# Optimization experiments

Hardware: AMD Instinct MI355X
Metric: run time of the kernel (lower is better)

## Reference

```python
import jax, jax.numpy as jnp
import numpy as np

D_MODEL = 1024
N_HEADS = 16
D_K = D_MODEL // N_HEADS  # 64
THETA = 10000.0


def _rope(x, token_positions):
    # x: [b, h, s, d], token_positions: [s]
    inv_freq = 1.0 / THETA ** (jnp.arange(0, D_K, 2, dtype=jnp.float32) / D_K)  # [d/2]
    ang = token_positions.astype(jnp.float32)[:, None] * inv_freq               # [s, d/2]
    cos, sin = jnp.cos(ang), jnp.sin(ang)                                       # broadcast over b,h
    x1 = x[..., 0::2]
    x2 = x[..., 1::2]
    even = x1 * cos - x2 * sin
    odd = x1 * sin + x2 * cos
    return jnp.stack([even, odd], axis=-1).reshape(x.shape)  # re-interleave


def setup_inputs() -> dict:
    key = jax.random.key(0)
    k1, k2, k3 = jax.random.split(key, 3)
    B, S = 2, 2048
    x = jax.random.normal(k1, (B, S, D_MODEL), dtype=jnp.float32)
    token_positions = jnp.arange(S, dtype=jnp.int32)
    std_qkv = np.sqrt(2.0 / (D_MODEL + 3 * D_MODEL))
    std_out = np.sqrt(2.0 / (D_MODEL + D_MODEL))
    W_qkv = jax.random.normal(k2, (3 * D_MODEL, D_MODEL), dtype=jnp.float32) * std_qkv
    W_out = jax.random.normal(k3, (D_MODEL, D_MODEL), dtype=jnp.float32) * std_out
    return {"x": x, "token_positions": token_positions, "W_qkv": W_qkv, "W_out": W_out}


def reference(x, token_positions, W_qkv, W_out):
    B, S, _ = x.shape
    qkv = jnp.einsum('bsi,oi->bso', x, W_qkv)                 # [b, s, 3*h*d]
    qkv = qkv.reshape(B, S, 3, N_HEADS, D_K)
    qkv = jnp.transpose(qkv, (2, 0, 3, 1, 4))                 # [3, b, h, s, d]
    q, k, v = qkv[0], qkv[1], qkv[2]
    q = _rope(q, token_positions)
    k = _rope(k, token_positions)
    scores = jnp.einsum('bhqd,bhkd->bhqk', q, k) / jnp.sqrt(jnp.float32(D_K))
    mask = jnp.tril(jnp.ones((S, S), dtype=bool))
    scores = jnp.where(mask, scores, -jnp.inf)
    attn = jax.nn.softmax(scores, axis=-1)
    out = jnp.einsum('bhqk,bhkd->bhqd', attn, v)              # [b, h, s, d]
    out = jnp.transpose(out, (0, 2, 1, 3)).reshape(B, S, D_MODEL)
    return jnp.einsum('bsi,oi->bso', out, W_out)
```

## Files before the change

kernel.cpp:

```cpp
#include <hip/hip_runtime.h>
#include <hip/hip_bf16.h>
#include <math.h>

#define D_MODEL 1024
#define N_HEADS 16
#define D_K     64
#define S_LEN   2048
#define B_SZ    2

typedef unsigned short u16;
typedef unsigned int   u32;
using short8  = __attribute__((ext_vector_type(8))) short;
using ushort8 = __attribute__((ext_vector_type(8))) unsigned short;
using f32x4   = __attribute__((ext_vector_type(4))) float;

__device__ inline float bf2f(u16 u) { return __uint_as_float((u32)u << 16); }
__device__ inline u16 f2bf(float f) {
    __hip_bfloat16 h = __float2bfloat16(f);
    return *(u16*)&h;
}
__device__ inline void gload_lds16(const void* g, void* l) {
    __builtin_amdgcn_global_load_lds(
        (const __attribute__((address_space(1))) unsigned int*)g,
        (__attribute__((address_space(3))) unsigned int*)l, 16, 0, 0);
}

__global__ __launch_bounds__(256)
void cast3_f32_bf16(const float* __restrict__ a, u16* __restrict__ ao, int na4,
                    const float* __restrict__ bsrc, u16* __restrict__ bo, int nb4,
                    const float* __restrict__ c, u16* __restrict__ co, int nc4) {
    int j = blockIdx.x * 256 + threadIdx.x;
    const float* src; u16* dst;
    if (j < na4) { src = a; dst = ao; }
    else {
        j -= na4;
        if (j < nb4) { src = bsrc; dst = bo; }
        else {
            j -= nb4;
            if (j >= nc4) return;
            src = c; dst = co;
        }
    }
    float4 v = ((const float4*)src)[j];
    ushort4 u;
    u.x = f2bf(v.x); u.y = f2bf(v.y); u.z = f2bf(v.z); u.w = f2bf(v.w);
    ((ushort4*)dst)[j] = u;
}

template <bool OUT_BF16>
__global__ __launch_bounds__(256)
void gemm_bt_mfma(const u16* __restrict__ A, const u16* __restrict__ B,
                  void* __restrict__ Cout, int M, int N, int K) {
    __shared__ u16 As[128 * 32];
    __shared__ u16 Bs[128 * 32];
    const int tid  = threadIdx.x;
    const int lane = tid & 63;
    const int wv   = tid >> 6;
    const int wm   = wv >> 1, wn = wv & 1;
    const int row0 = blockIdx.y * 128;
    const int col0 = blockIdx.x * 128;

    const int lr = lane >> 2;
    const int lc = (lane & 3) * 8;

    f32x4 acc[4][4] = {};

    for (int k0 = 0; k0 < K; k0 += 32) {
#pragma unroll
        for (int t = 0; t < 2; t++) {
            int rblk = wv * 32 + t * 16;
            gload_lds16(A + (size_t)(row0 + rblk + lr) * K + k0 + lc, &As[rblk * 32]);
            gload_lds16(B + (size_t)(col0 + rblk + lr) * K + k0 + lc, &Bs[rblk * 32]);
        }
        __syncthreads();

        short8 af[4], bfr[4];
#pragma unroll
        for (int mi = 0; mi < 4; mi++)
            af[mi] = *(const short8*)&As[(wm * 64 + mi * 16 + (lane & 15)) * 32 + (lane >> 4) * 8];
#pragma unroll
        for (int nj = 0; nj < 4; nj++)
            bfr[nj] = *(const short8*)&Bs[(wn * 64 + nj * 16 + (lane & 15)) * 32 + (lane >> 4) * 8];
#pragma unroll
        for (int mi = 0; mi < 4; mi++)
#pragma unroll
            for (int nj = 0; nj < 4; nj++)
                acc[mi][nj] = __builtin_amdgcn_mfma_f32_16x16x32_bf16(
                    af[mi], bfr[nj], acc[mi][nj], 0, 0, 0);
        __syncthreads();
    }

    const int cr = (lane >> 4) * 4;
    const int cc = lane & 15;
#pragma unroll
    for (int mi = 0; mi < 4; mi++) {
#pragma unroll
        for (int nj = 0; nj < 4; nj++) {
            int c = col0 + wn * 64 + nj * 16 + cc;
#pragma unroll
            for (int r = 0; r < 4; r++) {
                int rr = row0 + wm * 64 + mi * 16 + cr + r;
                if (OUT_BF16)
                    ((u16*)Cout)[(size_t)rr * N + c] = f2bf(acc[mi][nj][r]);
                else
                    ((float*)Cout)[(size_t)rr * N + c] = acc[mi][nj][r];
            }
        }
    }
}

__global__ __launch_bounds__(256)
void prep_vtrans_rope(u16* __restrict__ qkv, u16* __restrict__ VT,
                      const int* __restrict__ pos) {
    const int bid = blockIdx.x;
    const int tid = threadIdx.x;

    if (bid < 1024) {
        __shared__ u16 t[64][68];
        const int st = bid & 31, h = (bid >> 5) & 15, b = bid >> 9;
        const int bh = b * N_HEADS + h;
#pragma unroll
        for (int i = 0; i < 4; i++) {
            int e  = tid + i * 256;
            int sl = e >> 4;
            int c4 = e & 15;
            ushort4 v = *(const ushort4*)&qkv[((size_t)(b * S_LEN + st * 64 + sl) * 3 + 2) * D_MODEL
                                              + h * D_K + c4 * 4];
            *(ushort4*)&t[sl][c4 * 4] = v;
        }
        __syncthreads();
#pragma unroll
        for (int i = 0; i < 4; i++) {
            int e  = tid + i * 256;
            int d  = e >> 4;
            int s4 = e & 15;
            ushort4 o;
            o.x = t[s4 * 4 + 0][d];
            o.y = t[s4 * 4 + 1][d];
            o.z = t[s4 * 4 + 2][d];
            o.w = t[s4 * 4 + 3][d];
            *(ushort4*)&VT[((size_t)bh * D_K + d) * S_LEN + st * 64 + s4 * 4] = o;
        }
        return;
    }

    int e  = (bid - 1024) * 256 + tid;
    int j8 = e & 7;
    int h  = (e >> 3) & 15;
    int w  = (e >> 7) & 1;
    int s  = (e >> 8) & 2047;
    int b  = e >> 19;

    float p  = (float)pos[s];
    float sc = (w == 0) ? 0.125f : 1.0f;

    size_t base = (((size_t)(b * S_LEN + s) * 3 + w) * D_MODEL) + h * D_K + j8 * 8;
    ushort8 v = *(const ushort8*)&qkv[base];

    const float C = -0.41524101186092056f;
#pragma unroll
    for (int jj = 0; jj < 4; jj++) {
        int j = j8 * 4 + jj;
        float ang = p * exp2f((float)j * C);
        float sn, cs;
        __sincosf(ang, &sn, &cs);
        float x1 = bf2f(v[2 * jj]);
        float x2 = bf2f(v[2 * jj + 1]);
        v[2 * jj]     = f2bf((x1 * cs - x2 * sn) * sc);
        v[2 * jj + 1] = f2bf((x1 * sn + x2 * cs) * sc);
    }
    *(ushort8*)&qkv[base] = v;
}

__device__ __forceinline__ void attn_step(
    const u16* __restrict__ Ksc, const u16* __restrict__ Vsc,
    u16* __restrict__ Psw,
    short8 (&qf)[2], f32x4 (&acc)[4], float& mq, float& lq,
    int k0, int qw0, bool diag, int l15, int quad, int qsw)
{
    f32x4 s[4] = {};
    __builtin_amdgcn_s_setprio(1);
#pragma unroll
    for (int kf = 0; kf < 2; kf++)
#pragma unroll
        for (int nj = 0; nj < 4; nj++) {
            short8 kfr = *(const short8*)&Ksc[kf * 2048 + (nj * 16 + l15) * 32 + qsw * 8];
            s[nj] = __builtin_amdgcn_mfma_f32_16x16x32_bf16(kfr, qf[kf], s[nj], 0, 0, 0);
        }
    __builtin_amdgcn_s_setprio(0);

    if (diag) {
        const int row_g = qw0 + l15;
#pragma unroll
        for (int nj = 0; nj < 4; nj++)
#pragma unroll
            for (int r = 0; r < 4; r++) {
                int key_g = k0 + nj * 16 + quad * 4 + r;
                if (key_g > row_g) s[nj][r] = -INFINITY;
            }
    }

    float rmax = s[0][0];
#pragma unroll
    for (int nj = 0; nj < 4; nj++)
#pragma unroll
        for (int r = 0; r < 4; r++) rmax = fmaxf(rmax, s[nj][r]);
    rmax = fmaxf(rmax, __shfl_xor(rmax, 16, 64));
    rmax = fmaxf(rmax, __shfl_xor(rmax, 32, 64));

    if (!__all(rmax <= mq + 8.f)) {
        float mn = fmaxf(mq, rmax);
        float alpha = __expf(mq - mn);
        mq = mn;
        lq *= alpha;
#pragma unroll
        for (int nj = 0; nj < 4; nj++)
#pragma unroll
            for (int r = 0; r < 4; r++) acc[nj][r] *= alpha;
    }

    float rsum = 0.f;
#pragma unroll
    for (int nj = 0; nj < 4; nj++)
#pragma unroll
        for (int r = 0; r < 4; r++) {
            float p = __expf(s[nj][r] - mq);
            s[nj][r] = p;
            rsum += p;
        }
    rsum += __shfl_xor(rsum, 16, 64);
    rsum += __shfl_xor(rsum, 32, 64);
    lq += rsum;

#pragma unroll
    for (int nj = 0; nj < 4; nj++) {
        u32 lo = ((u32)f2bf(s[nj][1]) << 16) | f2bf(s[nj][0]);
        u32 hi = ((u32)f2bf(s[nj][3]) << 16) | f2bf(s[nj][2]);
        uint2 pk; pk.x = lo; pk.y = hi;
        *(uint2*)&Psw[l15 * 68 + nj * 16 + quad * 4] = pk;
    }

    __builtin_amdgcn_s_setprio(1);
#pragma unroll
    for (int kf = 0; kf < 2; kf++) {
        const u16* pp = &Psw[l15 * 68 + kf * 32 + quad * 8];
        uint2 plo = *(const uint2*)pp;
        uint2 phi = *(const uint2*)(pp + 4);
        u32 praw[4] = { plo.x, plo.y, phi.x, phi.y };
        short8 pf = *(const short8*)praw;
#pragma unroll
        for (int nj = 0; nj < 4; nj++) {
            short8 vf = *(const short8*)&Vsc[kf * 2048 + (nj * 16 + l15) * 32 + qsw * 8];
            acc[nj] = __builtin_amdgcn_mfma_f32_16x16x32_bf16(vf, pf, acc[nj], 0, 0, 0);
        }
    }
    __builtin_amdgcn_s_setprio(0);
}

__global__ __launch_bounds__(256)
void attn_mfma(const u16* __restrict__ qkv, const u16* __restrict__ VT,
               u16* __restrict__ out, float* __restrict__ partO,
               float* __restrict__ partML) {
    __shared__ u16 Ks[2][64 * 32];
    __shared__ u16 VsT[2][64 * 32];
    __shared__ u16 Ps[4][16 * 68];

    const int tid  = threadIdx.x;
    const int lane = tid & 63;
    const int wv   = tid >> 6;

    const int bid  = blockIdx.x;
    const int idx  = bid >> 3;
    const int bh   = (bid & 7) * 4 + (idx >> 5);
    const int rem  = idx & 31;
    const int pr   = rem >> 1;
    const int role = rem & 1;
    const int qtH  = 31 - pr;
    const int qtL  = pr;
    const int h    = bh & (N_HEADS - 1);
    const int b    = bh >> 4;

    const int l15  = lane & 15;
    const int quad = lane >> 4;
    const int qsw  = quad ^ ((l15 >> 1) & 3);
    const int qw0H = qtH * 64 + wv * 16;

    const size_t vtb = (size_t)bh * D_K * S_LEN;
    u16* Psw = &Ps[wv][0];
    const int lr  = lane >> 2;
    const int csw = ((lane & 3) ^ ((lane >> 3) & 3)) * 8;

    auto STAGE = [&](int kts) {
        const int k0s = kts * 64;
#pragma unroll
        for (int kf = 0; kf < 2; kf++)
            gload_lds16(qkv + ((size_t)(b * S_LEN + k0s + wv * 16 + lr) * 3 + 1) * D_MODEL
                            + h * D_K + kf * 32 + csw,
                        &Ks[kf][(wv * 16) * 32]);
#pragma unroll
        for (int kc = 0; kc < 2; kc++)
            gload_lds16(VT + vtb + (size_t)(wv * 16 + lr) * S_LEN + k0s + kc * 32 + csw,
                        &VsT[kc][(wv * 16) * 32]);
    };

    short8 qfH[2];
#pragma unroll
    for (int kf = 0; kf < 2; kf++)
        qfH[kf] = *(const short8*)&qkv[((size_t)(b * S_LEN + qw0H + l15) * 3 + 0) * D_MODEL
                                       + h * D_K + kf * 32 + quad * 8];
    f32x4 accH[4] = {};
    float mqH = -INFINITY, lqH = 0.f;

    const int kbeg = role ? 17 : 0;
    const int kend = role ? qtH : 16;
    for (int kt = kbeg; kt <= kend; kt++) {
        STAGE(kt);
        __syncthreads();
        attn_step(&Ks[0][0], &VsT[0][0], Psw, qfH, accH, mqH, lqH,
                  kt * 64, qw0H, kt == qtH, l15, quad, qsw);
        __syncthreads();
    }

    {
        const size_t unit = (size_t)(bh * 16 + (qtH - 16)) * 2 + role;
        float* Od = partO + unit * 4096 + (size_t)(wv * 16 + l15) * 64;
#pragma unroll
        for (int nj = 0; nj < 4; nj++)
            *(f32x4*)&Od[nj * 16 + quad * 4] = accH[nj];
        if (quad == 0) {
            float* ML = partML + unit * 128;
            ML[wv * 16 + l15]      = mqH;
            ML[64 + wv * 16 + l15] = lqH;
        }
    }

    if (!role) return;

    const int qw0L = qtL * 64 + wv * 16;
    short8 qfL[2];
#pragma unroll
    for (int kf = 0; kf < 2; kf++)
        qfL[kf] = *(const short8*)&qkv[((size_t)(b * S_LEN + qw0L + l15) * 3 + 0) * D_MODEL
                                       + h * D_K + kf * 32 + quad * 8];
    f32x4 accL[4] = {};
    float mqL = -INFINITY, lqL = 0.f;

    for (int kt = 0; kt <= qtL; kt++) {
        STAGE(kt);
        __syncthreads();
        attn_step(&Ks[0][0], &VsT[0][0], Psw, qfL, accL, mqL, lqL,
                  kt * 64, qw0L, kt == qtL, l15, quad, qsw);
        __syncthreads();
    }

    float invl = 1.f / lqL;
#pragma unroll
    for (int nj = 0; nj < 4; nj++) {
        ushort4 o;
        o.x = f2bf(accL[nj][0] * invl); o.y = f2bf(accL[nj][1] * invl);
        o.z = f2bf(accL[nj][2] * invl); o.w = f2bf(accL[nj][3] * invl);
        *(ushort4*)&out[(size_t)(b * S_LEN + qw0L + l15) * D_MODEL
                        + h * D_K + nj * 16 + quad * 4] = o;
    }
}

__global__ __launch_bounds__(256)
void attn_combine(const float* __restrict__ partO, const float* __restrict__ partML,
                  u16* __restrict__ out) {
    const int t16 = blockIdx.x & 15;
    const int bh  = blockIdx.x >> 4;
    const int h = bh & (N_HEADS - 1), b = bh >> 4;
    const int q0 = (t16 + 16) * 64;
    const int tid = threadIdx.x;
    const int q  = tid >> 2;
    const int d0 = (tid & 3) * 16;

    const size_t u0 = (size_t)(bh * 16 + t16) * 2;
    const float* O0 = partO + u0 * 4096;
    const float* O1 = O0 + 4096;
    const float* ML0 = partML + u0 * 128;
    const float* ML1 = ML0 + 128;

    float m0 = ML0[q], l0 = ML0[64 + q];
    float m1 = ML1[q], l1 = ML1[64 + q];
    float ms = fmaxf(m0, m1);
    float f0 = __expf(m0 - ms), f1 = __expf(m1 - ms);
    float inv = 1.f / (l0 * f0 + l1 * f1);
    f0 *= inv; f1 *= inv;
#pragma unroll
    for (int i = 0; i < 4; i++) {
        float4 a = *(const float4*)&O0[q * 64 + d0 + i * 4];
        float4 c = *(const float4*)&O1[q * 64 + d0 + i * 4];
        ushort4 o;
        o.x = f2bf(a.x * f0 + c.x * f1);
        o.y = f2bf(a.y * f0 + c.y * f1);
        o.z = f2bf(a.z * f0 + c.z * f1);
        o.w = f2bf(a.w * f0 + c.w * f1);
        *(ushort4*)&out[(size_t)(b * S_LEN + q0 + q) * D_MODEL + h * D_K + d0 + i * 4] = o;
    }
}

extern "C" void kernel_launch(void* const* d_in, const int* in_sizes, int n_in,
                              void* d_out, int out_size, void* d_ws, size_t ws_size,
                              hipStream_t stream) {
    const float* x    = (const float*)d_in[0];
    const int*   pos  = (const int*)d_in[1];
    const float* Wqkv = (const float*)d_in[2];
    const float* Wout = (const float*)d_in[3];
    float*       out  = (float*)d_out;

    const int M = B_SZ * S_LEN;

    u16* qkvb = (u16*)d_ws;
    u16* aob  = qkvb + (size_t)M * 3 * D_MODEL;
    u16* xb   = aob  + (size_t)M * D_MODEL;
    u16* wqb  = xb   + (size_t)M * D_MODEL;
    u16* wob  = wqb  + (size_t)3 * D_MODEL * D_MODEL;
    u16* vtb  = wob  + (size_t)D_MODEL * D_MODEL;
    float* partO  = (float*)(vtb + (size_t)M * D_MODEL);
    float* partML = partO + (size_t)1024 * 4096;

    const int na4 = M * D_MODEL / 4;
    const int nb4 = 3 * D_MODEL * D_MODEL / 4;
    const int nc4 = D_MODEL * D_MODEL / 4;
    cast3_f32_bf16<<<(na4 + nb4 + nc4 + 255) / 256, 256, 0, stream>>>(
        x, xb, na4, Wqkv, wqb, nb4, Wout, wob, nc4);

    gemm_bt_mfma<true><<<dim3(3 * D_MODEL / 128, M / 128), 256, 0, stream>>>(
        xb, wqb, qkvb, M, 3 * D_MODEL, D_MODEL);

    prep_vtrans_rope<<<5120, 256, 0, stream>>>(qkvb, vtb, pos);

    attn_mfma<<<1024, 256, 0, stream>>>(qkvb, vtb, aob, partO, partML);
    attn_combine<<<512, 256, 0, stream>>>(partO, partML, aob);

    gemm_bt_mfma<false><<<dim3(D_MODEL / 128, M / 128), 256, 0, stream>>>(
        aob, wob, out, M, D_MODEL, D_MODEL);
}
```

Baseline: 197.6 us.

## Prefetch K/V tiles via registers, use exp2 softmax, smaller-tile output GEMM

The attention loop now prefetches the next K and V tiles into registers while computing the current tile, then writes them to LDS, instead of staging synchronously before each step. Softmax switches to base-2 exponentials, with the log2(e) factor folded into the Q scale, and the rescale threshold is raised from 8 to 12. The output projection uses a new 64-row tile GEMM to launch more blocks. These target load latency, exp cost and occupancy, at the cost of more registers and an extra barrier per iteration.

```diff
diff --git a/kernel.cpp b/kernel.cpp
--- a/kernel.cpp
+++ b/kernel.cpp
@@ -19,6 +19,7 @@
     __hip_bfloat16 h = __float2bfloat16(f);
     return *(u16*)&h;
 }
+__device__ inline float fast_exp2(float x) { return __builtin_amdgcn_exp2f(x); }
 __device__ inline void gload_lds16(const void* g, void* l) {
     __builtin_amdgcn_global_load_lds(
         (const __attribute__((address_space(1))) unsigned int*)g,
@@ -110,6 +111,64 @@
 }
 
 __global__ __launch_bounds__(256)
+void gemm_bt_mfma_64r(const u16* __restrict__ A, const u16* __restrict__ B,
+                      float* __restrict__ Cout, int M, int N, int K) {
+    __shared__ u16 As[64 * 32];
+    __shared__ u16 Bs[128 * 32];
+    const int tid  = threadIdx.x;
+    const int lane = tid & 63;
+    const int wv   = tid >> 6;
+    const int wm   = wv >> 1, wn = wv & 1;
+    const int row0 = blockIdx.y * 64;
+    const int col0 = blockIdx.x * 128;
+
+    const int lr = lane >> 2;
+    const int lc = (lane & 3) * 8;
+
+    f32x4 acc[2][4] = {};
+
+    for (int k0 = 0; k0 < K; k0 += 32) {
+        gload_lds16(A + (size_t)(row0 + wv * 16 + lr) * K + k0 + lc, &As[(wv * 16) * 32]);
+#pragma unroll
+        for (int t = 0; t < 2; t++) {
+            int rblk = wv * 32 + t * 16;
+            gload_lds16(B + (size_t)(col0 + rblk + lr) * K + k0 + lc, &Bs[rblk * 32]);
+        }
+        __syncthreads();
+
+        short8 af[2], bfr[4];
+#pragma unroll
+        for (int mi = 0; mi < 2; mi++)
+            af[mi] = *(const short8*)&As[(wm * 32 + mi * 16 + (lane & 15)) * 32 + (lane >> 4) * 8];
+#pragma unroll
+        for (int nj = 0; nj < 4; nj++)
+            bfr[nj] = *(const short8*)&Bs[(wn * 64 + nj * 16 + (lane & 15)) * 32 + (lane >> 4) * 8];
+#pragma unroll
+        for (int mi = 0; mi < 2; mi++)
+#pragma unroll
+            for (int nj = 0; nj < 4; nj++)
+                acc[mi][nj] = __builtin_amdgcn_mfma_f32_16x16x32_bf16(
+                    af[mi], bfr[nj], acc[mi][nj], 0, 0, 0);
+        __syncthreads();
+    }
+
+    const int cr = (lane >> 4) * 4;
+    const int cc = lane & 15;
+#pragma unroll
+    for (int mi = 0; mi < 2; mi++) {
+#pragma unroll
+        for (int nj = 0; nj < 4; nj++) {
+            int c = col0 + wn * 64 + nj * 16 + cc;
+#pragma unroll
+            for (int r = 0; r < 4; r++) {
+                int rr = row0 + wm * 32 + mi * 16 + cr + r;
+                Cout[(size_t)rr * N + c] = acc[mi][nj][r];
+            }
+        }
+    }
+}
+
+__global__ __launch_bounds__(256)
 void prep_vtrans_rope(u16* __restrict__ qkv, u16* __restrict__ VT,
                       const int* __restrict__ pos) {
     const int bid = blockIdx.x;
@@ -152,7 +211,7 @@
     int b  = e >> 19;
 
     float p  = (float)pos[s];
-    float sc = (w == 0) ? 0.125f : 1.0f;
+    float sc = (w == 0) ? 0.18033688011112042f : 1.0f;
 
     size_t base = (((size_t)(b * S_LEN + s) * 3 + w) * D_MODEL) + h * D_K + j8 * 8;
     ushort8 v = *(const ushort8*)&qkv[base];
@@ -161,7 +220,7 @@
 #pragma unroll
     for (int jj = 0; jj < 4; jj++) {
         int j = j8 * 4 + jj;
-        float ang = p * exp2f((float)j * C);
+        float ang = p * fast_exp2((float)j * C);
         float sn, cs;
         __sincosf(ang, &sn, &cs);
         float x1 = bf2f(v[2 * jj]);
@@ -208,9 +267,9 @@
     rmax = fmaxf(rmax, __shfl_xor(rmax, 16, 64));
     rmax = fmaxf(rmax, __shfl_xor(rmax, 32, 64));
 
-    if (!__all(rmax <= mq + 8.f)) {
+    if (!__all(rmax <= mq + 12.f)) {
         float mn = fmaxf(mq, rmax);
-        float alpha = __expf(mq - mn);
+        float alpha = fast_exp2(mq - mn);
         mq = mn;
         lq *= alpha;
 #pragma unroll
@@ -224,7 +283,7 @@
     for (int nj = 0; nj < 4; nj++)
 #pragma unroll
         for (int r = 0; r < 4; r++) {
-            float p = __expf(s[nj][r] - mq);
+            float p = fast_exp2(s[nj][r] - mq);
             s[nj][r] = p;
             rsum += p;
         }
@@ -303,6 +362,26 @@
                         &VsT[kc][(wv * 16) * 32]);
     };
 
+    ushort8 kreg[2], vreg[2];
+    auto REGLOAD = [&](int kts) {
+        const int k0s = kts * 64;
+#pragma unroll
+        for (int kf = 0; kf < 2; kf++)
+            kreg[kf] = *(const ushort8*)&qkv[((size_t)(b * S_LEN + k0s + wv * 16 + lr) * 3 + 1) * D_MODEL
+                                             + h * D_K + kf * 32 + csw];
+#pragma unroll
+        for (int kc = 0; kc < 2; kc++)
+            vreg[kc] = *(const ushort8*)&VT[vtb + (size_t)(wv * 16 + lr) * S_LEN + k0s + kc * 32 + csw];
+    };
+    auto LDSW = [&]() {
+#pragma unroll
+        for (int kf = 0; kf < 2; kf++)
+            *(ushort8*)&Ks[kf][(wv * 16) * 32 + lane * 8] = kreg[kf];
+#pragma unroll
+        for (int kc = 0; kc < 2; kc++)
+            *(ushort8*)&VsT[kc][(wv * 16) * 32 + lane * 8] = vreg[kc];
+    };
+
     short8 qfH[2];
 #pragma unroll
     for (int kf = 0; kf < 2; kf++)
@@ -313,12 +392,17 @@
 
     const int kbeg = role ? 17 : 0;
     const int kend = role ? qtH : 16;
-    for (int kt = kbeg; kt <= kend; kt++) {
-        STAGE(kt);
-        __syncthreads();
-        attn_step(&Ks[0][0], &VsT[0][0], Psw, qfH, accH, mqH, lqH,
-                  kt * 64, qw0H, kt == qtH, l15, quad, qsw);
-        __syncthreads();
+    if (kbeg <= kend) {
+        STAGE(kbeg);
+        __syncthreads();
+        for (int kt = kbeg; kt <= kend; kt++) {
+            const bool more = kt < kend;
+            if (more) REGLOAD(kt + 1);
+            attn_step(&Ks[0][0], &VsT[0][0], Psw, qfH, accH, mqH, lqH,
+                      kt * 64, qw0H, kt == qtH, l15, quad, qsw);
+            __syncthreads();
+            if (more) { LDSW(); __syncthreads(); }
+        }
     }
 
     {
@@ -345,12 +429,15 @@
     f32x4 accL[4] = {};
     float mqL = -INFINITY, lqL = 0.f;
 
+    STAGE(0);
+    __syncthreads();
     for (int kt = 0; kt <= qtL; kt++) {
-        STAGE(kt);
-        __syncthreads();
+        const bool more = kt < qtL;
+        if (more) REGLOAD(kt + 1);
         attn_step(&Ks[0][0], &VsT[0][0], Psw, qfL, accL, mqL, lqL,
                   kt * 64, qw0L, kt == qtL, l15, quad, qsw);
         __syncthreads();
+        if (more) { LDSW(); __syncthreads(); }
     }
 
     float invl = 1.f / lqL;
@@ -384,7 +471,7 @@
     float m0 = ML0[q], l0 = ML0[64 + q];
     float m1 = ML1[q], l1 = ML1[64 + q];
     float ms = fmaxf(m0, m1);
-    float f0 = __expf(m0 - ms), f1 = __expf(m1 - ms);
+    float f0 = fast_exp2(m0 - ms), f1 = fast_exp2(m1 - ms);
     float inv = 1.f / (l0 * f0 + l1 * f1);
     f0 *= inv; f1 *= inv;
 #pragma unroll
@@ -434,6 +521,6 @@
     attn_mfma<<<1024, 256, 0, stream>>>(qkvb, vtb, aob, partO, partML);
     attn_combine<<<512, 256, 0, stream>>>(partO, partML, aob);
 
-    gemm_bt_mfma<false><<<dim3(D_MODEL / 128, M / 128), 256, 0, stream>>>(
+    gemm_bt_mfma_64r<<<dim3(D_MODEL / 128, M / 64), 256, 0, stream>>>(
         aob, wob, out, M, D_MODEL, D_MODEL);
 }
```

After: 191.3 us. -3.2%, faster.
